# Kernel tuning notes

Measured on AMD Instinct MI355X. Metric: run time of the kernel, lower is better.

## Reference

```python
import jax, jax.numpy as jnp
import numpy as np

B, S, D = 2, 2048, 1024
E = 4
H = 4 * D  # MLP hidden; SwiGLU w_v outputs 2*H


def setup_inputs() -> dict:
    key = jax.random.key(0)
    k_x, k_r, k_wv, k_wp = jax.random.split(key, 4)
    x = jax.random.normal(k_x, (B, S, D), dtype=jnp.float32)
    w_router = jax.random.normal(k_r, (D, E), dtype=jnp.float32) * 0.02
    # stacked expert weights, stored [in, out] (transpose of torch Linear)
    w_v = jax.random.normal(k_wv, (E, D, 2 * H), dtype=jnp.float32) * 0.02
    w_proj = jax.random.normal(k_wp, (E, H, D), dtype=jnp.float32) * 0.02
    return {"x": x, "w_router": w_router, "w_v": w_v, "w_proj": w_proj}


def reference(x, w_router, w_v, w_proj):
    # router: softmax then argmax (top-1); output NOT scaled by prob (matches torch src)
    logits = jnp.einsum("bsd,de->bse", x, w_router)
    probs = jax.nn.softmax(logits, axis=-1)
    expert_idx = jnp.argmax(probs, axis=-1)  # [B,S]
    # dense per-expert SwiGLU MLP: gv [E,B,S,2H]
    gv = jnp.einsum("bsd,edh->ebsh", x, w_v)
    gate_raw, value = jnp.split(gv, 2, axis=-1)
    h = gate_raw * jax.nn.sigmoid(gate_raw) * value  # beta=1.0 SiLU gate
    y = jnp.einsum("ebsh,ehd->ebsd", h, w_proj)  # [E,B,S,D]
    onehot = jax.nn.one_hot(expert_idx, w_v.shape[0], dtype=x.dtype)  # [B,S,E]
    return jnp.einsum("bse,ebsd->bsd", onehot, y)
```

## Files before the change

kernel.cpp:

```cpp
#include <hip/hip_runtime.h>


#define TTOK 4096
#define DIN  1024
#define HDIM 4096
#define H2   8192
#define TPAD 4608
#define LDK  40

typedef float f32x4 __attribute__((ext_vector_type(4)));
typedef __bf16 bf16x8 __attribute__((ext_vector_type(8)));
typedef unsigned short u16x8 __attribute__((ext_vector_type(8)));
typedef unsigned short u16x4 __attribute__((ext_vector_type(4)));

__device__ __forceinline__ unsigned short f2b(float f) {
  unsigned int u = __builtin_bit_cast(unsigned int, f);
  u += 0x7fffu + ((u >> 16) & 1u);
  return (unsigned short)(u >> 16);
}

__global__ __launch_bounds__(256) void k_router(const float* __restrict__ x,
    const float* __restrict__ wrt, int* __restrict__ eidx,
    int* __restrict__ rank, int* __restrict__ cnt) {
  const int w = threadIdx.x >> 6, lane = threadIdx.x & 63;
  const int t = blockIdx.x * 4 + w;
  const float* xr = x + (size_t)t * DIN;
  const float4* w4 = (const float4*)wrt;
  float a0 = 0.f, a1 = 0.f, a2 = 0.f, a3 = 0.f;
  for (int k = 0; k < DIN; k += 64) {
    float xv = xr[k + lane];
    float4 ww = w4[k + lane];
    a0 += xv * ww.x; a1 += xv * ww.y; a2 += xv * ww.z; a3 += xv * ww.w;
  }
  #pragma unroll
  for (int off = 32; off; off >>= 1) {
    a0 += __shfl_xor(a0, off); a1 += __shfl_xor(a1, off);
    a2 += __shfl_xor(a2, off); a3 += __shfl_xor(a3, off);
  }
  if (lane == 0) {
    int e = 0; float b = a0;
    if (a1 > b) { b = a1; e = 1; }
    if (a2 > b) { b = a2; e = 2; }
    if (a3 > b) { b = a3; e = 3; }
    eidx[t] = e;
    rank[t] = atomicAdd(&cnt[e], 1);
  }
}

__global__ void k_setup(const int* __restrict__ cnt, int* __restrict__ poff,
                        int* __restrict__ tExp, int* __restrict__ tRow,
                        int* __restrict__ nMt) {
  int p = 0, nm = 0;
  for (int e = 0; e < 4; e++) {
    poff[e] = p;
    int mt = (cnt[e] + 127) >> 7;
    for (int i = 0; i < mt; i++) { tExp[nm] = e; tRow[nm] = p + i * 128; nm++; }
    p += mt * 128;
  }
  poff[4] = p;
  *nMt = nm;
}

__global__ __launch_bounds__(256) void k_scatter(const int* __restrict__ eidx,
    const int* __restrict__ rank, const int* __restrict__ poff,
    int* __restrict__ perm) {
  const int t = blockIdx.x * 256 + threadIdx.x;
  const int pos = poff[eidx[t]] + rank[t];
  perm[pos] = t;
}

__global__ __launch_bounds__(256) void k_gather(const float* __restrict__ x,
    const int* __restrict__ perm, unsigned short* __restrict__ A) {
  const int r = blockIdx.x;
  const int t = perm[r];
  unsigned short* dst = A + (size_t)r * DIN + threadIdx.x * 4;
  if (t < 0) {
    u16x4 z{0, 0, 0, 0};
    *(u16x4*)dst = z;
  } else {
    float4 v = *(const float4*)(x + (size_t)t * DIN + threadIdx.x * 4);
    u16x4 o{f2b(v.x), f2b(v.y), f2b(v.z), f2b(v.w)};
    *(u16x4*)dst = o;
  }
}

__global__ __launch_bounds__(256) void k_gemm1(const unsigned short* __restrict__ A,
    const float* __restrict__ wv, unsigned short* __restrict__ Hb,
    const int* __restrict__ tExp, const int* __restrict__ tRow,
    const int* __restrict__ nMt) {
  if ((int)blockIdx.y >= *nMt) return;
  __shared__ __align__(16) unsigned short As[128 * LDK];
  __shared__ __align__(16) unsigned short Bg[128 * LDK];
  __shared__ __align__(16) unsigned short Bv[128 * LDK];
  const int e = tExp[blockIdx.y];
  const int row0 = tRow[blockIdx.y];
  const int n0 = blockIdx.x * 128;
  const int tid = threadIdx.x;
  const int lane = tid & 63;
  const int w = tid >> 6, wr = w >> 1, wc = w & 1;

  f32x4 accg[4][4], accv[4][4];
  #pragma unroll
  for (int i = 0; i < 4; i++)
    #pragma unroll
    for (int j = 0; j < 4; j++) {
      accg[i][j] = f32x4{0.f, 0.f, 0.f, 0.f};
      accv[i][j] = f32x4{0.f, 0.f, 0.f, 0.f};
    }

  const int arow = tid >> 1;
  const int ak = (tid & 1) * 16;
  const unsigned short* aSrc = A + (size_t)(row0 + arow) * DIN + ak;
  const int t128 = tid & 127;
  const int bA = t128 & 31;
  const int bKg = t128 >> 5;
  const float* bSrc = wv + (size_t)e * DIN * H2 + n0 + (tid < 128 ? 0 : HDIM);
  unsigned short* bDst = (tid < 128) ? Bg : Bv;

  const int krow = (lane >> 4) * 8;
  const int mrow = lane & 15;

  for (int k0 = 0; k0 < DIN; k0 += 32) {
    u16x8 a0 = *(const u16x8*)(aSrc + k0);
    u16x8 a1 = *(const u16x8*)(aSrc + k0 + 8);
    const float* srow = bSrc + (size_t)(k0 + bKg * 8) * H2;
    *(u16x8*)&As[arow * LDK + ak] = a0;
    *(u16x8*)&As[arow * LDK + ak + 8] = a1;
    #pragma unroll
    for (int c = 0; c < 4; c++) {
      const int n = bA + 32 * c;
      const float* s = srow + n;
      u16x8 pk;
      #pragma unroll
      for (int r = 0; r < 8; r++) pk[r] = f2b(s[(size_t)r * H2]);
      *(u16x8*)&bDst[n * LDK + bKg * 8] = pk;
    }
    __syncthreads();
    u16x8 af[4];
    #pragma unroll
    for (int fm = 0; fm < 4; fm++)
      af[fm] = *(const u16x8*)&As[(wr * 64 + fm * 16 + mrow) * LDK + krow];
    #pragma unroll
    for (int fn = 0; fn < 4; fn++) {
      u16x8 bg = *(const u16x8*)&Bg[(wc * 64 + fn * 16 + mrow) * LDK + krow];
      u16x8 bv = *(const u16x8*)&Bv[(wc * 64 + fn * 16 + mrow) * LDK + krow];
      #pragma unroll
      for (int fm = 0; fm < 4; fm++) {
        accg[fm][fn] = __builtin_amdgcn_mfma_f32_16x16x32_bf16(
            __builtin_bit_cast(bf16x8, af[fm]), __builtin_bit_cast(bf16x8, bg),
            accg[fm][fn], 0, 0, 0);
        accv[fm][fn] = __builtin_amdgcn_mfma_f32_16x16x32_bf16(
            __builtin_bit_cast(bf16x8, af[fm]), __builtin_bit_cast(bf16x8, bv),
            accv[fm][fn], 0, 0, 0);
      }
    }
    __syncthreads();
  }
  #pragma unroll
  for (int fm = 0; fm < 4; fm++) {
    const int rbase = row0 + wr * 64 + fm * 16 + (lane >> 4) * 4;
    #pragma unroll
    for (int fn = 0; fn < 4; fn++) {
      const int col = n0 + wc * 64 + fn * 16 + mrow;
      #pragma unroll
      for (int j = 0; j < 4; j++) {
        float g = accg[fm][fn][j];
        float v = accv[fm][fn][j];
        float h = g / (1.f + __expf(-g)) * v;
        Hb[(size_t)(rbase + j) * HDIM + col] = f2b(h);
      }
    }
  }
}

__global__ __launch_bounds__(256) void k_gemm2(const unsigned short* __restrict__ Hb,
    const float* __restrict__ wp, float* __restrict__ out,
    const int* __restrict__ tExp, const int* __restrict__ tRow,
    const int* __restrict__ nMt, const int* __restrict__ perm) {
  if ((int)blockIdx.y >= *nMt) return;
  __shared__ __align__(16) unsigned short As[128 * LDK];
  __shared__ __align__(16) unsigned short Bs[128 * LDK];
  const int e = tExp[blockIdx.y];
  const int row0 = tRow[blockIdx.y];
  const int n0 = blockIdx.x * 128;
  const int tid = threadIdx.x;
  const int lane = tid & 63;
  const int w = tid >> 6, wr = w >> 1, wc = w & 1;
  f32x4 acc[4][4];
  #pragma unroll
  for (int i = 0; i < 4; i++)
    #pragma unroll
    for (int j = 0; j < 4; j++) acc[i][j] = f32x4{0.f, 0.f, 0.f, 0.f};

  const int t128 = tid & 127;
  const int bA = t128 & 31, bKg = t128 >> 5;
  const float* bSrc = wp + (size_t)e * HDIM * DIN + n0;
  const unsigned short* aSrc = Hb + (size_t)(row0 + t128) * HDIM;
  const int krow = (lane >> 4) * 8, mrow = lane & 15;

  for (int k0 = 0; k0 < HDIM; k0 += 32) {
    if (tid < 128) {
      #pragma unroll
      for (int q = 0; q < 4; q++) {
        u16x8 v = *(const u16x8*)(aSrc + k0 + q * 8);
        *(u16x8*)&As[t128 * LDK + q * 8] = v;
      }
    } else {
      const float* srow = bSrc + (size_t)(k0 + bKg * 8) * DIN;
      #pragma unroll
      for (int c = 0; c < 4; c++) {
        const int n = bA + 32 * c;
        const float* s = srow + n;
        u16x8 pk;
        #pragma unroll
        for (int r = 0; r < 8; r++) pk[r] = f2b(s[(size_t)r * DIN]);
        *(u16x8*)&Bs[n * LDK + bKg * 8] = pk;
      }
    }
    __syncthreads();
    u16x8 af[4];
    #pragma unroll
    for (int fm = 0; fm < 4; fm++)
      af[fm] = *(const u16x8*)&As[(wr * 64 + fm * 16 + mrow) * LDK + krow];
    #pragma unroll
    for (int fn = 0; fn < 4; fn++) {
      u16x8 bf = *(const u16x8*)&Bs[(wc * 64 + fn * 16 + mrow) * LDK + krow];
      #pragma unroll
      for (int fm = 0; fm < 4; fm++)
        acc[fm][fn] = __builtin_amdgcn_mfma_f32_16x16x32_bf16(
            __builtin_bit_cast(bf16x8, af[fm]), __builtin_bit_cast(bf16x8, bf),
            acc[fm][fn], 0, 0, 0);
    }
    __syncthreads();
  }
  #pragma unroll
  for (int fm = 0; fm < 4; fm++) {
    const int rbase = row0 + wr * 64 + fm * 16 + (lane >> 4) * 4;
    #pragma unroll
    for (int fn = 0; fn < 4; fn++) {
      const int col = n0 + wc * 64 + fn * 16 + mrow;
      #pragma unroll
      for (int j = 0; j < 4; j++) {
        const int t = perm[rbase + j];
        if (t >= 0) out[(size_t)t * DIN + col] = acc[fm][fn][j];
      }
    }
  }
}

extern "C" void kernel_launch(void* const* d_in, const int* in_sizes, int n_in,
                              void* d_out, int out_size, void* d_ws, size_t ws_size,
                              hipStream_t stream) {
  const float* x        = (const float*)d_in[0];
  const float* w_router = (const float*)d_in[1];
  const float* w_v      = (const float*)d_in[2];
  const float* w_proj   = (const float*)d_in[3];
  float* out = (float*)d_out;
  char* ws = (char*)d_ws;

  int* cnt  = (int*)(ws + 0);
  int* nMt  = (int*)(ws + 16);
  int* poff = (int*)(ws + 32);
  int* tExp = (int*)(ws + 128);
  int* tRow = (int*)(ws + 320);
  int* eidx = (int*)(ws + 512);
  int* rank = (int*)(ws + 512 + 16384);
  int* perm = (int*)(ws + 512 + 32768);
  unsigned short* Abuf = (unsigned short*)(ws + 52224);
  unsigned short* Hbuf = (unsigned short*)(ws + 52224 + 9437184);

  hipMemsetAsync(cnt, 0, 16, stream);
  hipMemsetAsync(perm, 0xFF, TPAD * 4, stream);
  k_router<<<TTOK / 4, 256, 0, stream>>>(x, w_router, eidx, rank, cnt);
  k_setup<<<1, 1, 0, stream>>>(cnt, poff, tExp, tRow, nMt);
  k_scatter<<<TTOK / 256, 256, 0, stream>>>(eidx, rank, poff, perm);
  k_gather<<<TPAD, 256, 0, stream>>>(x, perm, Abuf);
  k_gemm1<<<dim3(HDIM / 128, 36), 256, 0, stream>>>(Abuf, w_v, Hbuf, tExp, tRow, nMt);
  k_gemm2<<<dim3(DIN / 128, 36), 256, 0, stream>>>(Hbuf, w_proj, out, tExp, tRow, nMt, perm);
}
```

Before: 685.6 us.

## Pre-transpose weights to bf16, use direct global-to-LDS loads, split-K gemm2

```diff
diff --git a/kernel.cpp b/kernel.cpp
--- a/kernel.cpp
+++ b/kernel.cpp
@@ -6,7 +6,6 @@
 #define HDIM 4096
 #define H2   8192
 #define TPAD 4608
-#define LDK  40
 
 typedef float f32x4 __attribute__((ext_vector_type(4)));
 typedef __bf16 bf16x8 __attribute__((ext_vector_type(8)));
@@ -17,6 +16,12 @@
   unsigned int u = __builtin_bit_cast(unsigned int, f);
   u += 0x7fffu + ((u >> 16) & 1u);
   return (unsigned short)(u >> 16);
+}
+
+__device__ __forceinline__ void gload16(const void* g, void* l) {
+  __builtin_amdgcn_global_load_lds(
+      (const __attribute__((address_space(1))) unsigned int*)g,
+      (__attribute__((address_space(3))) unsigned int*)l, 16, 0, 0);
 }
 
 __global__ __launch_bounds__(256) void k_router(const float* __restrict__ x,
@@ -84,20 +89,53 @@
   }
 }
 
+__global__ __launch_bounds__(256) void k_transpose(const float* __restrict__ src,
+    unsigned short* __restrict__ dst, int K, int N) {
+  __shared__ __align__(16) unsigned short T[64][72];
+  const int n0 = blockIdx.x * 64, k0 = blockIdx.y * 64;
+  const size_t eoff = (size_t)blockIdx.z * K * N;
+  const int tid = threadIdx.x;
+  const int rr = tid >> 4;
+  const int cc = (tid & 15) * 4;
+  #pragma unroll
+  for (int i = 0; i < 4; i++) {
+    const int r = rr + i * 16;
+    float4 v = *(const float4*)(src + eoff + (size_t)(k0 + r) * N + n0 + cc);
+    T[cc + 0][r] = f2b(v.x);
+    T[cc + 1][r] = f2b(v.y);
+    T[cc + 2][r] = f2b(v.z);
+    T[cc + 3][r] = f2b(v.w);
+  }
+  __syncthreads();
+  const int n = tid >> 2, kc = (tid & 3) * 16;
+  u16x8 a = *(const u16x8*)&T[n][kc];
+  u16x8 b = *(const u16x8*)&T[n][kc + 8];
+  unsigned short* dp = dst + eoff + (size_t)(n0 + n) * K + k0 + kc;
+  *(u16x8*)(dp) = a;
+  *(u16x8*)(dp + 8) = b;
+}
+
 __global__ __launch_bounds__(256) void k_gemm1(const unsigned short* __restrict__ A,
-    const float* __restrict__ wv, unsigned short* __restrict__ Hb,
+    const unsigned short* __restrict__ Wt, unsigned short* __restrict__ Hb,
     const int* __restrict__ tExp, const int* __restrict__ tRow,
     const int* __restrict__ nMt) {
   if ((int)blockIdx.y >= *nMt) return;
-  __shared__ __align__(16) unsigned short As[128 * LDK];
-  __shared__ __align__(16) unsigned short Bg[128 * LDK];
-  __shared__ __align__(16) unsigned short Bv[128 * LDK];
+  __shared__ __align__(16) unsigned short As[128 * 32];
+  __shared__ __align__(16) unsigned short Bg[128 * 32];
+  __shared__ __align__(16) unsigned short Bv[128 * 32];
   const int e = tExp[blockIdx.y];
   const int row0 = tRow[blockIdx.y];
   const int n0 = blockIdx.x * 128;
-  const int tid = threadIdx.x;
-  const int lane = tid & 63;
+  const int tid = threadIdx.x, lane = tid & 63;
   const int w = tid >> 6, wr = w >> 1, wc = w & 1;
+  const int rl = lane >> 2;
+  const int kc = (lane & 3) * 8;
+  const int mrow = lane & 15, krow = (lane >> 4) * 8;
+
+  const unsigned short* aG  = A  + (size_t)(row0 + w * 16 + rl) * DIN + kc;
+  const unsigned short* bgG = Wt + (size_t)e * H2 * DIN
+                                 + (size_t)(n0 + w * 16 + rl) * DIN + kc;
+  const unsigned short* bvG = bgG + (size_t)HDIM * DIN;
 
   f32x4 accg[4][4], accv[4][4];
   #pragma unroll
@@ -108,52 +146,32 @@
       accv[i][j] = f32x4{0.f, 0.f, 0.f, 0.f};
     }
 
-  const int arow = tid >> 1;
-  const int ak = (tid & 1) * 16;
-  const unsigned short* aSrc = A + (size_t)(row0 + arow) * DIN + ak;
-  const int t128 = tid & 127;
-  const int bA = t128 & 31;
-  const int bKg = t128 >> 5;
-  const float* bSrc = wv + (size_t)e * DIN * H2 + n0 + (tid < 128 ? 0 : HDIM);
-  unsigned short* bDst = (tid < 128) ? Bg : Bv;
-
-  const int krow = (lane >> 4) * 8;
-  const int mrow = lane & 15;
-
   for (int k0 = 0; k0 < DIN; k0 += 32) {
-    u16x8 a0 = *(const u16x8*)(aSrc + k0);
-    u16x8 a1 = *(const u16x8*)(aSrc + k0 + 8);
-    const float* srow = bSrc + (size_t)(k0 + bKg * 8) * H2;
-    *(u16x8*)&As[arow * LDK + ak] = a0;
-    *(u16x8*)&As[arow * LDK + ak + 8] = a1;
-    #pragma unroll
-    for (int c = 0; c < 4; c++) {
-      const int n = bA + 32 * c;
-      const float* s = srow + n;
-      u16x8 pk;
-      #pragma unroll
-      for (int r = 0; r < 8; r++) pk[r] = f2b(s[(size_t)r * H2]);
-      *(u16x8*)&bDst[n * LDK + bKg * 8] = pk;
-    }
-    __syncthreads();
-    u16x8 af[4];
-    #pragma unroll
-    for (int fm = 0; fm < 4; fm++)
-      af[fm] = *(const u16x8*)&As[(wr * 64 + fm * 16 + mrow) * LDK + krow];
-    #pragma unroll
-    for (int fn = 0; fn < 4; fn++) {
-      u16x8 bg = *(const u16x8*)&Bg[(wc * 64 + fn * 16 + mrow) * LDK + krow];
-      u16x8 bv = *(const u16x8*)&Bv[(wc * 64 + fn * 16 + mrow) * LDK + krow];
+    gload16(aG + k0,                     &As[w * 512]);
+    gload16(aG + k0 + (size_t)64 * DIN,  &As[w * 512 + 2048]);
+    gload16(bgG + k0,                    &Bg[w * 512]);
+    gload16(bgG + k0 + (size_t)64 * DIN, &Bg[w * 512 + 2048]);
+    gload16(bvG + k0,                    &Bv[w * 512]);
+    gload16(bvG + k0 + (size_t)64 * DIN, &Bv[w * 512 + 2048]);
+    __syncthreads();
+    u16x8 af[4], bg[4], bv[4];
+    #pragma unroll
+    for (int f = 0; f < 4; f++) {
+      af[f] = *(const u16x8*)&As[(wr * 64 + f * 16 + mrow) * 32 + krow];
+      bg[f] = *(const u16x8*)&Bg[(wc * 64 + f * 16 + mrow) * 32 + krow];
+      bv[f] = *(const u16x8*)&Bv[(wc * 64 + f * 16 + mrow) * 32 + krow];
+    }
+    #pragma unroll
+    for (int fn = 0; fn < 4; fn++)
       #pragma unroll
       for (int fm = 0; fm < 4; fm++) {
         accg[fm][fn] = __builtin_amdgcn_mfma_f32_16x16x32_bf16(
-            __builtin_bit_cast(bf16x8, af[fm]), __builtin_bit_cast(bf16x8, bg),
+            __builtin_bit_cast(bf16x8, af[fm]), __builtin_bit_cast(bf16x8, bg[fn]),
             accg[fm][fn], 0, 0, 0);
         accv[fm][fn] = __builtin_amdgcn_mfma_f32_16x16x32_bf16(
-            __builtin_bit_cast(bf16x8, af[fm]), __builtin_bit_cast(bf16x8, bv),
+            __builtin_bit_cast(bf16x8, af[fm]), __builtin_bit_cast(bf16x8, bv[fn]),
             accv[fm][fn], 0, 0, 0);
       }
-    }
     __syncthreads();
   }
   #pragma unroll
@@ -174,63 +192,50 @@
 }
 
 __global__ __launch_bounds__(256) void k_gemm2(const unsigned short* __restrict__ Hb,
-    const float* __restrict__ wp, float* __restrict__ out,
+    const unsigned short* __restrict__ Wt, float* __restrict__ out,
     const int* __restrict__ tExp, const int* __restrict__ tRow,
     const int* __restrict__ nMt, const int* __restrict__ perm) {
-  if ((int)blockIdx.y >= *nMt) return;
-  __shared__ __align__(16) unsigned short As[128 * LDK];
-  __shared__ __align__(16) unsigned short Bs[128 * LDK];
-  const int e = tExp[blockIdx.y];
-  const int row0 = tRow[blockIdx.y];
+  const int my = blockIdx.y >> 1;
+  const int ks = blockIdx.y & 1;
+  if (my >= *nMt) return;
+  __shared__ __align__(16) unsigned short As[128 * 32];
+  __shared__ __align__(16) unsigned short Bs[128 * 32];
+  const int e = tExp[my];
+  const int row0 = tRow[my];
   const int n0 = blockIdx.x * 128;
-  const int tid = threadIdx.x;
-  const int lane = tid & 63;
+  const int tid = threadIdx.x, lane = tid & 63;
   const int w = tid >> 6, wr = w >> 1, wc = w & 1;
+  const int rl = lane >> 2, kc = (lane & 3) * 8;
+  const int mrow = lane & 15, krow = (lane >> 4) * 8;
+
+  const unsigned short* aG = Hb + (size_t)(row0 + w * 16 + rl) * HDIM + ks * 2048 + kc;
+  const unsigned short* bG = Wt + (size_t)e * DIN * HDIM
+                                + (size_t)(n0 + w * 16 + rl) * HDIM + ks * 2048 + kc;
   f32x4 acc[4][4];
   #pragma unroll
   for (int i = 0; i < 4; i++)
     #pragma unroll
     for (int j = 0; j < 4; j++) acc[i][j] = f32x4{0.f, 0.f, 0.f, 0.f};
 
-  const int t128 = tid & 127;
-  const int bA = t128 & 31, bKg = t128 >> 5;
-  const float* bSrc = wp + (size_t)e * HDIM * DIN + n0;
-  const unsigned short* aSrc = Hb + (size_t)(row0 + t128) * HDIM;
-  const int krow = (lane >> 4) * 8, mrow = lane & 15;
-
-  for (int k0 = 0; k0 < HDIM; k0 += 32) {
-    if (tid < 128) {
-      #pragma unroll
-      for (int q = 0; q < 4; q++) {
-        u16x8 v = *(const u16x8*)(aSrc + k0 + q * 8);
-        *(u16x8*)&As[t128 * LDK + q * 8] = v;
-      }
-    } else {
-      const float* srow = bSrc + (size_t)(k0 + bKg * 8) * DIN;
-      #pragma unroll
-      for (int c = 0; c < 4; c++) {
-        const int n = bA + 32 * c;
-        const float* s = srow + n;
-        u16x8 pk;
-        #pragma unroll
-        for (int r = 0; r < 8; r++) pk[r] = f2b(s[(size_t)r * DIN]);
-        *(u16x8*)&Bs[n * LDK + bKg * 8] = pk;
-      }
-    }
-    __syncthreads();
-    u16x8 af[4];
-    #pragma unroll
-    for (int fm = 0; fm < 4; fm++)
-      af[fm] = *(const u16x8*)&As[(wr * 64 + fm * 16 + mrow) * LDK + krow];
-    #pragma unroll
-    for (int fn = 0; fn < 4; fn++) {
-      u16x8 bf = *(const u16x8*)&Bs[(wc * 64 + fn * 16 + mrow) * LDK + krow];
+  for (int k0 = 0; k0 < 2048; k0 += 32) {
+    gload16(aG + k0,                      &As[w * 512]);
+    gload16(aG + k0 + (size_t)64 * HDIM,  &As[w * 512 + 2048]);
+    gload16(bG + k0,                      &Bs[w * 512]);
+    gload16(bG + k0 + (size_t)64 * HDIM,  &Bs[w * 512 + 2048]);
+    __syncthreads();
+    u16x8 af[4], bf[4];
+    #pragma unroll
+    for (int f = 0; f < 4; f++) {
+      af[f] = *(const u16x8*)&As[(wr * 64 + f * 16 + mrow) * 32 + krow];
+      bf[f] = *(const u16x8*)&Bs[(wc * 64 + f * 16 + mrow) * 32 + krow];
+    }
+    #pragma unroll
+    for (int fn = 0; fn < 4; fn++)
       #pragma unroll
       for (int fm = 0; fm < 4; fm++)
         acc[fm][fn] = __builtin_amdgcn_mfma_f32_16x16x32_bf16(
-            __builtin_bit_cast(bf16x8, af[fm]), __builtin_bit_cast(bf16x8, bf),
+            __builtin_bit_cast(bf16x8, af[fm]), __builtin_bit_cast(bf16x8, bf[fn]),
             acc[fm][fn], 0, 0, 0);
-    }
     __syncthreads();
   }
   #pragma unroll
@@ -242,7 +247,7 @@
       #pragma unroll
       for (int j = 0; j < 4; j++) {
         const int t = perm[rbase + j];
-        if (t >= 0) out[(size_t)t * DIN + col] = acc[fm][fn][j];
+        if (t >= 0) atomicAdd(&out[(size_t)t * DIN + col], acc[fm][fn][j]);
       }
     }
   }
@@ -267,14 +272,19 @@
   int* rank = (int*)(ws + 512 + 16384);
   int* perm = (int*)(ws + 512 + 32768);
   unsigned short* Abuf = (unsigned short*)(ws + 52224);
-  unsigned short* Hbuf = (unsigned short*)(ws + 52224 + 9437184);
+  unsigned short* Hbuf = (unsigned short*)(ws + 9489408);
+  unsigned short* Wvt  = (unsigned short*)(ws + 47238144);
+  unsigned short* Wpt  = (unsigned short*)(ws + 114347008);
 
   hipMemsetAsync(cnt, 0, 16, stream);
   hipMemsetAsync(perm, 0xFF, TPAD * 4, stream);
+  hipMemsetAsync(out, 0, (size_t)out_size * 4, stream);
   k_router<<<TTOK / 4, 256, 0, stream>>>(x, w_router, eidx, rank, cnt);
   k_setup<<<1, 1, 0, stream>>>(cnt, poff, tExp, tRow, nMt);
   k_scatter<<<TTOK / 256, 256, 0, stream>>>(eidx, rank, poff, perm);
   k_gather<<<TPAD, 256, 0, stream>>>(x, perm, Abuf);
-  k_gemm1<<<dim3(HDIM / 128, 36), 256, 0, stream>>>(Abuf, w_v, Hbuf, tExp, tRow, nMt);
-  k_gemm2<<<dim3(DIN / 128, 36), 256, 0, stream>>>(Hbuf, w_proj, out, tExp, tRow, nMt, perm);
-}
+  k_transpose<<<dim3(H2 / 64, DIN / 64, 4), 256, 0, stream>>>(w_v, Wvt, DIN, H2);
+  k_transpose<<<dim3(DIN / 64, HDIM / 64, 4), 256, 0, stream>>>(w_proj, Wpt, HDIM, DIN);
+  k_gemm1<<<dim3(HDIM / 128, 36), 256, 0, stream>>>(Abuf, Wvt, Hbuf, tExp, tRow, nMt);
+  k_gemm2<<<dim3(DIN / 128, 72), 256, 0, stream>>>(Hbuf, Wpt, out, tExp, tRow, nMt, perm);
+}
```

Result: faster. 599.5 us (-12.6%).
